# Kernel optimization log

Hardware: AMD Instinct MI355X
Metric: run time of the kernel (lower is better)

Reference implementation:

```python
import jax, jax.numpy as jnp
import numpy as np

SIGMA_AGG = 0.5
SIGMA_DIS = 3.0
ALPHA = 0.5
BETA = 0.25
EPS = 1e-5
K_MAX = 8  # number of kernel/text instances per image; labels in {0..K_MAX}, 0 = background


def setup_inputs() -> dict:
    key = jax.random.key(0)
    ks = jax.random.split(key, 7)
    B, C, H, W = 16, 4, 640, 640
    return dict(
        pred_regions=jax.random.normal(ks[0], (B, 1, H, W), jnp.float32),
        regions_gt=jax.random.randint(ks[1], (B, 1, H, W), 0, 2).astype(jnp.float32),
        pred_kernels=jax.random.normal(ks[2], (B, 1, H, W), jnp.float32),
        kernels_gt=jax.random.randint(ks[3], (B, 1, H, W), 0, 2).astype(jnp.float32),
        pred_similarities=jax.random.normal(ks[4], (B, C, H, W), jnp.float32),
        text_mask_ndi_labels=jax.random.randint(ks[5], (B, H, W), 0, K_MAX + 1, dtype=jnp.int32),
        kernel_mask_ndi_labels=jax.random.randint(ks[6], (B, H, W), 0, K_MAX + 1, dtype=jnp.int32),
    )


def _dice_loss(pred, gt, eps):
    # sigmoid -> per-sample dice, summed over batch (matches Text/KernelDiceLoss)
    p = jax.nn.sigmoid(pred).reshape(pred.shape[0], -1)
    g = gt.reshape(gt.shape[0], -1)
    inter = jnp.sum(p * g, axis=1)
    denom = (jnp.sum(p * p, axis=1) + eps) + (jnp.sum(g * g, axis=1) + eps)
    dice = (2.0 * inter + eps) / denom
    return jnp.sum(1.0 - dice)


def _agg_dis_single(sim, tlab, klab):
    # sim: (C, H, W); tlab/klab: (H, W) int instance labels (0 = background)
    C = sim.shape[0]
    sim = sim.reshape(C, -1)
    tlab = tlab.reshape(-1)
    klab = klab.reshape(-1)
    nseg = K_MAX + 1

    s2 = jnp.sum(sim * sim, axis=0)  # per-pixel squared feature norm, (N,)
    ones = jnp.ones_like(s2)
    ck = jax.ops.segment_sum(ones, klab, num_segments=nseg)  # kernel cardinalities
    ct = jax.ops.segment_sum(ones, tlab, num_segments=nseg)  # text cardinalities

    # Aggregation: || sim*1[T==i] - sim*1[K==i]/(ck_i+1) ||_F per instance i.
    # Per pixel, nonzero only for i = tlab[p] or i = klab[p]:
    inv = 1.0 / (ck + 1.0)
    same = tlab == klab
    coef_t = jnp.where(same, (1.0 - inv[klab]) ** 2, 1.0)  # contributes to instance tlab
    coef_k = jnp.where(same, 0.0, inv[klab] ** 2)          # contributes to instance klab
    n2 = (jax.ops.segment_sum(s2 * coef_t, tlab, num_segments=nseg)
          + jax.ops.segment_sum(s2 * coef_k, klab, num_segments=nseg))
    norm = jnp.sqrt(n2[1:])  # drop background segment 0
    # NOTE: torch.max(scalar, 0)[0] on a 0-d tensor is identity (no clamp) - reproduced here.
    l_agg = jnp.sum(jnp.log((norm - SIGMA_AGG) ** 2 + 1.0) / (ct[1:] + 1.0))

    # Discrimination: kernel masks are disjoint, so
    # ||mu_i - mu_j||_F^2 = a_i + a_j with a_i = sum_{K==i} s2 / (ck_i + 0.001)^2
    a = jax.ops.segment_sum(s2, klab, num_segments=nseg)[1:] / (ck[1:] + 0.001) ** 2
    pair = SIGMA_DIS - jnp.sqrt(a[:, None] + a[None, :])
    val = jnp.log(pair ** 2 + 1.0)
    triu = jnp.triu(jnp.ones((K_MAX, K_MAX), bool), 1)
    l_dis = jnp.sum(jnp.where(triu, val, 0.0)) / (K_MAX * (K_MAX - 1))
    return l_agg, l_dis


def reference(pred_regions, regions_gt, pred_kernels, kernels_gt,
              pred_similarities, text_mask_ndi_labels, kernel_mask_ndi_labels):
    # OHEM mask is computed in the torch code but never used by TextDiceLoss, so it is omitted.
    loss_regions = _dice_loss(pred_regions, regions_gt, EPS)
    loss_kernel = _dice_loss(pred_kernels, kernels_gt, EPS)
    l_agg, l_dis = jax.vmap(_agg_dis_single)(pred_similarities,
                                             text_mask_ndi_labels,
                                             kernel_mask_ndi_labels)
    loss_aggregation = jnp.sum(l_agg)
    loss_discrimination = jnp.sum(l_dis)
    loss = loss_regions + ALPHA * loss_kernel + BETA * (loss_aggregation + loss_discrimination)
    return (loss, loss_regions, loss_kernel, loss_aggregation, loss_discrimination)
```

## Files before the change

kernel.cpp:

```cpp
#include <hip/hip_runtime.h>
#include <math.h>


#define NSEG 9
#define NACC 51
#define NBATCH 16
#define EPSF 1e-5f

__device__ __forceinline__ float wave_reduce_sum(float v) {
#pragma unroll
    for (int off = 32; off > 0; off >>= 1)
        v += __shfl_down(v, off, 64);
    return v;
}

__device__ __forceinline__ float sigm(float x) {
    return 1.0f / (1.0f + __expf(-x));
}

__global__ __launch_bounds__(256) void pan_main(
    const float* __restrict__ pred_r, const float* __restrict__ gt_r,
    const float* __restrict__ pred_k, const float* __restrict__ gt_k,
    const float* __restrict__ sim,
    const int* __restrict__ tlab, const int* __restrict__ klab,
    float* __restrict__ ws, int npix)
{
    const int b = blockIdx.y;
    const int nvec = npix >> 2;
    const long long base = (long long)b * npix;
    const long long sbase = (long long)b * 4 * npix;

    const float4* pr4 = (const float4*)(pred_r + base);
    const float4* gr4 = (const float4*)(gt_r + base);
    const float4* pk4 = (const float4*)(pred_k + base);
    const float4* gk4 = (const float4*)(gt_k + base);
    const float4* c0_4 = (const float4*)(sim + sbase);
    const float4* c1_4 = (const float4*)(sim + sbase + npix);
    const float4* c2_4 = (const float4*)(sim + sbase + 2LL * npix);
    const float4* c3_4 = (const float4*)(sim + sbase + 3LL * npix);
    const int4* tl4 = (const int4*)(tlab + base);
    const int4* kl4 = (const int4*)(klab + base);

    float ctA[NSEG], ckA[NSEG], StA[NSEG], SkA[NSEG], SsA[NSEG];
#pragma unroll
    for (int s = 0; s < NSEG; ++s) {
        ctA[s] = 0.0f; ckA[s] = 0.0f; StA[s] = 0.0f; SkA[s] = 0.0f; SsA[s] = 0.0f;
    }
    float rpg = 0.0f, rpp = 0.0f, rgg = 0.0f;
    float kpg = 0.0f, kpp = 0.0f, kgg = 0.0f;

    for (int i = blockIdx.x * blockDim.x + threadIdx.x; i < nvec;
         i += gridDim.x * blockDim.x) {
        float4 pr = pr4[i], gr = gr4[i], pk = pk4[i], gk = gk4[i];
        float4 c0 = c0_4[i], c1 = c1_4[i], c2 = c2_4[i], c3 = c3_4[i];
        int4 tl = tl4[i], kl = kl4[i];

        {
            float p;
            p = sigm(pr.x); rpg += p * gr.x; rpp += p * p; rgg += gr.x * gr.x;
            p = sigm(pr.y); rpg += p * gr.y; rpp += p * p; rgg += gr.y * gr.y;
            p = sigm(pr.z); rpg += p * gr.z; rpp += p * p; rgg += gr.z * gr.z;
            p = sigm(pr.w); rpg += p * gr.w; rpp += p * p; rgg += gr.w * gr.w;
        }
        {
            float p;
            p = sigm(pk.x); kpg += p * gk.x; kpp += p * p; kgg += gk.x * gk.x;
            p = sigm(pk.y); kpg += p * gk.y; kpp += p * p; kgg += gk.y * gk.y;
            p = sigm(pk.z); kpg += p * gk.z; kpp += p * p; kgg += gk.z * gk.z;
            p = sigm(pk.w); kpg += p * gk.w; kpp += p * p; kgg += gk.w * gk.w;
        }

        float s2x = c0.x * c0.x + c1.x * c1.x + c2.x * c2.x + c3.x * c3.x;
        float s2y = c0.y * c0.y + c1.y * c1.y + c2.y * c2.y + c3.y * c3.y;
        float s2z = c0.z * c0.z + c1.z * c1.z + c2.z * c2.z + c3.z * c3.z;
        float s2w = c0.w * c0.w + c1.w * c1.w + c2.w * c2.w + c3.w * c3.w;

#pragma unroll
        for (int s = 0; s < NSEG; ++s) {
            {
                bool t = (tl.x == s), k = (kl.x == s);
                ctA[s] += t ? 1.0f : 0.0f;
                ckA[s] += k ? 1.0f : 0.0f;
                StA[s] += t ? s2x : 0.0f;
                SkA[s] += k ? s2x : 0.0f;
                SsA[s] += (t && k) ? s2x : 0.0f;
            }
            {
                bool t = (tl.y == s), k = (kl.y == s);
                ctA[s] += t ? 1.0f : 0.0f;
                ckA[s] += k ? 1.0f : 0.0f;
                StA[s] += t ? s2y : 0.0f;
                SkA[s] += k ? s2y : 0.0f;
                SsA[s] += (t && k) ? s2y : 0.0f;
            }
            {
                bool t = (tl.z == s), k = (kl.z == s);
                ctA[s] += t ? 1.0f : 0.0f;
                ckA[s] += k ? 1.0f : 0.0f;
                StA[s] += t ? s2z : 0.0f;
                SkA[s] += k ? s2z : 0.0f;
                SsA[s] += (t && k) ? s2z : 0.0f;
            }
            {
                bool t = (tl.w == s), k = (kl.w == s);
                ctA[s] += t ? 1.0f : 0.0f;
                ckA[s] += k ? 1.0f : 0.0f;
                StA[s] += t ? s2w : 0.0f;
                SkA[s] += k ? s2w : 0.0f;
                SsA[s] += (t && k) ? s2w : 0.0f;
            }
        }
    }

    __shared__ float red[4][NACC];
    const int lane = threadIdx.x & 63;
    const int wv = threadIdx.x >> 6;

#pragma unroll
    for (int s = 0; s < NSEG; ++s) {
        float r;
        r = wave_reduce_sum(ctA[s]); if (lane == 0) red[wv][s] = r;
        r = wave_reduce_sum(ckA[s]); if (lane == 0) red[wv][NSEG + s] = r;
        r = wave_reduce_sum(StA[s]); if (lane == 0) red[wv][2 * NSEG + s] = r;
        r = wave_reduce_sum(SkA[s]); if (lane == 0) red[wv][3 * NSEG + s] = r;
        r = wave_reduce_sum(SsA[s]); if (lane == 0) red[wv][4 * NSEG + s] = r;
    }
    {
        float r;
        r = wave_reduce_sum(rpg); if (lane == 0) red[wv][45] = r;
        r = wave_reduce_sum(rpp); if (lane == 0) red[wv][46] = r;
        r = wave_reduce_sum(rgg); if (lane == 0) red[wv][47] = r;
        r = wave_reduce_sum(kpg); if (lane == 0) red[wv][48] = r;
        r = wave_reduce_sum(kpp); if (lane == 0) red[wv][49] = r;
        r = wave_reduce_sum(kgg); if (lane == 0) red[wv][50] = r;
    }
    __syncthreads();
    if (threadIdx.x < NACC) {
        float s = red[0][threadIdx.x] + red[1][threadIdx.x] +
                  red[2][threadIdx.x] + red[3][threadIdx.x];
        atomicAdd(&ws[b * NACC + threadIdx.x], s);
    }
}

__global__ __launch_bounds__(64) void pan_finalize(
    const float* __restrict__ ws, float* __restrict__ out)
{
    const int b = threadIdx.x;
    float dice_r = 0.0f, dice_k = 0.0f, lagg = 0.0f, ldis = 0.0f;

    if (b < NBATCH) {
        const float* w = ws + b * NACC;
        {
            float pg = w[45], pp = w[46], gg = w[47];
            dice_r = 1.0f - (2.0f * pg + EPSF) / ((pp + EPSF) + (gg + EPSF));
            pg = w[48]; pp = w[49]; gg = w[50];
            dice_k = 1.0f - (2.0f * pg + EPSF) / ((pp + EPSF) + (gg + EPSF));
        }
        float a[8];
#pragma unroll
        for (int i = 1; i < NSEG; ++i) {
            float ct = w[i], ck = w[NSEG + i];
            float St = w[2 * NSEG + i], Sk = w[3 * NSEG + i], Ss = w[4 * NSEG + i];
            float inv = 1.0f / (ck + 1.0f);
            float omi = 1.0f - inv;
            float n2 = omi * omi * Ss + (St - Ss) + inv * inv * (Sk - Ss);
            float nrm = sqrtf(n2);
            float d = nrm - 0.5f;
            lagg += logf(d * d + 1.0f) / (ct + 1.0f);
            float ckd = ck + 0.001f;
            a[i - 1] = Sk / (ckd * ckd);
        }
#pragma unroll
        for (int i = 0; i < 8; ++i) {
#pragma unroll
            for (int j = i + 1; j < 8; ++j) {
                float pair = 3.0f - sqrtf(a[i] + a[j]);
                ldis += logf(pair * pair + 1.0f);
            }
        }
        ldis *= (1.0f / 56.0f);
    }

    dice_r = wave_reduce_sum(dice_r);
    dice_k = wave_reduce_sum(dice_k);
    lagg = wave_reduce_sum(lagg);
    ldis = wave_reduce_sum(ldis);

    if (threadIdx.x == 0) {
        float loss = dice_r + 0.5f * dice_k + 0.25f * (lagg + ldis);
        out[0] = loss;
        out[1] = dice_r;
        out[2] = dice_k;
        out[3] = lagg;
        out[4] = ldis;
    }
}

extern "C" void kernel_launch(void* const* d_in, const int* in_sizes, int n_in,
                              void* d_out, int out_size, void* d_ws, size_t ws_size,
                              hipStream_t stream) {
    const float* pred_r = (const float*)d_in[0];
    const float* gt_r   = (const float*)d_in[1];
    const float* pred_k = (const float*)d_in[2];
    const float* gt_k   = (const float*)d_in[3];
    const float* sim    = (const float*)d_in[4];
    const int*   tlab   = (const int*)d_in[5];
    const int*   klab   = (const int*)d_in[6];
    float* out = (float*)d_out;
    float* ws  = (float*)d_ws;

    const int npix = in_sizes[0] / NBATCH;

    hipMemsetAsync(ws, 0, NBATCH * NACC * sizeof(float), stream);

    dim3 grid(128, NBATCH);
    pan_main<<<grid, 256, 0, stream>>>(pred_r, gt_r, pred_k, gt_k, sim,
                                       tlab, klab, ws, npix);
    pan_finalize<<<1, 64, 0, stream>>>(ws, out);
}
```

Measured before the change: 288.5 us.

## Replace per-segment register accumulation with per-thread LDS histogram bins

Drops the unrolled nine-segment compare-and-select loop that updated 45 register accumulators for every pixel. Each pixel now does five indexed atomic adds into a per-thread column of a 45×256 shared-memory bin array. The bins are reduced per wave at the end and added straight into the workspace. The grid x-dimension also drops from 128 to 100 blocks per image. This cuts the per-pixel ALU work and register pressure, but each block now uses about 46 KB of LDS, which limits how many blocks fit on a CU and adds LDS atomic traffic.

```diff
diff --git a/kernel.cpp b/kernel.cpp
--- a/kernel.cpp
+++ b/kernel.cpp
@@ -6,6 +6,7 @@
 #define NACC 51
 #define NBATCH 16
 #define EPSF 1e-5f
+#define GX 100
 
 __device__ __forceinline__ float wave_reduce_sum(float v) {
 #pragma unroll
@@ -25,7 +26,16 @@
     const int* __restrict__ tlab, const int* __restrict__ klab,
     float* __restrict__ ws, int npix)
 {
+    __shared__ float bins[45 * 256];
+
+    const int tid = threadIdx.x;
     const int b = blockIdx.y;
+
+#pragma unroll
+    for (int q = 0; q < 45; ++q)
+        bins[q * 256 + tid] = 0.0f;
+    __syncthreads();
+
     const int nvec = npix >> 2;
     const long long base = (long long)b * npix;
     const long long sbase = (long long)b * 4 * npix;
@@ -41,15 +51,21 @@
     const int4* tl4 = (const int4*)(tlab + base);
     const int4* kl4 = (const int4*)(klab + base);
 
-    float ctA[NSEG], ckA[NSEG], StA[NSEG], SkA[NSEG], SsA[NSEG];
-#pragma unroll
-    for (int s = 0; s < NSEG; ++s) {
-        ctA[s] = 0.0f; ckA[s] = 0.0f; StA[s] = 0.0f; SkA[s] = 0.0f; SsA[s] = 0.0f;
-    }
     float rpg = 0.0f, rpp = 0.0f, rgg = 0.0f;
     float kpg = 0.0f, kpp = 0.0f, kgg = 0.0f;
 
-    for (int i = blockIdx.x * blockDim.x + threadIdx.x; i < nvec;
+#define DO_PIX(TL, KL, S2) {                                   \
+        float s2m = ((TL) == (KL)) ? (S2) : 0.0f;              \
+        float* bt = bins + (TL) * 256 + tid;                   \
+        float* bk = bins + (KL) * 256 + tid;                   \
+        atomicAdd(bt, 1.0f);                         \
+        atomicAdd(bk + 9 * 256, 1.0f);               \
+        atomicAdd(bt + 18 * 256, (S2));              \
+        atomicAdd(bk + 27 * 256, (S2));              \
+        atomicAdd(bt + 36 * 256, s2m);               \
+    }
+
+    for (int i = blockIdx.x * blockDim.x + tid; i < nvec;
          i += gridDim.x * blockDim.x) {
         float4 pr = pr4[i], gr = gr4[i], pk = pk4[i], gk = gk4[i];
         float4 c0 = c0_4[i], c1 = c1_4[i], c2 = c2_4[i], c3 = c3_4[i];
@@ -61,9 +77,6 @@
             p = sigm(pr.y); rpg += p * gr.y; rpp += p * p; rgg += gr.y * gr.y;
             p = sigm(pr.z); rpg += p * gr.z; rpp += p * p; rgg += gr.z * gr.z;
             p = sigm(pr.w); rpg += p * gr.w; rpp += p * p; rgg += gr.w * gr.w;
-        }
-        {
-            float p;
             p = sigm(pk.x); kpg += p * gk.x; kpp += p * p; kgg += gk.x * gk.x;
             p = sigm(pk.y); kpg += p * gk.y; kpp += p * p; kgg += gk.y * gk.y;
             p = sigm(pk.z); kpg += p * gk.z; kpp += p * p; kgg += gk.z * gk.z;
@@ -75,71 +88,32 @@
         float s2z = c0.z * c0.z + c1.z * c1.z + c2.z * c2.z + c3.z * c3.z;
         float s2w = c0.w * c0.w + c1.w * c1.w + c2.w * c2.w + c3.w * c3.w;
 
-#pragma unroll
-        for (int s = 0; s < NSEG; ++s) {
-            {
-                bool t = (tl.x == s), k = (kl.x == s);
-                ctA[s] += t ? 1.0f : 0.0f;
-                ckA[s] += k ? 1.0f : 0.0f;
-                StA[s] += t ? s2x : 0.0f;
-                SkA[s] += k ? s2x : 0.0f;
-                SsA[s] += (t && k) ? s2x : 0.0f;
-            }
-            {
-                bool t = (tl.y == s), k = (kl.y == s);
-                ctA[s] += t ? 1.0f : 0.0f;
-                ckA[s] += k ? 1.0f : 0.0f;
-                StA[s] += t ? s2y : 0.0f;
-                SkA[s] += k ? s2y : 0.0f;
-                SsA[s] += (t && k) ? s2y : 0.0f;
-            }
-            {
-                bool t = (tl.z == s), k = (kl.z == s);
-                ctA[s] += t ? 1.0f : 0.0f;
-                ckA[s] += k ? 1.0f : 0.0f;
-                StA[s] += t ? s2z : 0.0f;
-                SkA[s] += k ? s2z : 0.0f;
-                SsA[s] += (t && k) ? s2z : 0.0f;
-            }
-            {
-                bool t = (tl.w == s), k = (kl.w == s);
-                ctA[s] += t ? 1.0f : 0.0f;
-                ckA[s] += k ? 1.0f : 0.0f;
-                StA[s] += t ? s2w : 0.0f;
-                SkA[s] += k ? s2w : 0.0f;
-                SsA[s] += (t && k) ? s2w : 0.0f;
-            }
-        }
+        DO_PIX(tl.x, kl.x, s2x);
+        DO_PIX(tl.y, kl.y, s2y);
+        DO_PIX(tl.z, kl.z, s2z);
+        DO_PIX(tl.w, kl.w, s2w);
+    }
+#undef DO_PIX
+
+    __syncthreads();
+
+    const int lane = tid & 63;
+    const int wv = tid >> 6;
+
+    for (int q = wv; q < 45; q += 4) {
+        const float4 v = *(const float4*)&bins[q * 256 + (lane << 2)];
+        float s = (v.x + v.y) + (v.z + v.w);
+        s = wave_reduce_sum(s);
+        if (lane == 0) atomicAdd(&ws[b * NACC + q], s);
     }
 
-    __shared__ float red[4][NACC];
-    const int lane = threadIdx.x & 63;
-    const int wv = threadIdx.x >> 6;
-
-#pragma unroll
-    for (int s = 0; s < NSEG; ++s) {
-        float r;
-        r = wave_reduce_sum(ctA[s]); if (lane == 0) red[wv][s] = r;
-        r = wave_reduce_sum(ckA[s]); if (lane == 0) red[wv][NSEG + s] = r;
-        r = wave_reduce_sum(StA[s]); if (lane == 0) red[wv][2 * NSEG + s] = r;
-        r = wave_reduce_sum(SkA[s]); if (lane == 0) red[wv][3 * NSEG + s] = r;
-        r = wave_reduce_sum(SsA[s]); if (lane == 0) red[wv][4 * NSEG + s] = r;
-    }
-    {
-        float r;
-        r = wave_reduce_sum(rpg); if (lane == 0) red[wv][45] = r;
-        r = wave_reduce_sum(rpp); if (lane == 0) red[wv][46] = r;
-        r = wave_reduce_sum(rgg); if (lane == 0) red[wv][47] = r;
-        r = wave_reduce_sum(kpg); if (lane == 0) red[wv][48] = r;
-        r = wave_reduce_sum(kpp); if (lane == 0) red[wv][49] = r;
-        r = wave_reduce_sum(kgg); if (lane == 0) red[wv][50] = r;
-    }
-    __syncthreads();
-    if (threadIdx.x < NACC) {
-        float s = red[0][threadIdx.x] + red[1][threadIdx.x] +
-                  red[2][threadIdx.x] + red[3][threadIdx.x];
-        atomicAdd(&ws[b * NACC + threadIdx.x], s);
-    }
+    float r;
+    r = wave_reduce_sum(rpg); if (lane == 0) atomicAdd(&ws[b * NACC + 45], r);
+    r = wave_reduce_sum(rpp); if (lane == 0) atomicAdd(&ws[b * NACC + 46], r);
+    r = wave_reduce_sum(rgg); if (lane == 0) atomicAdd(&ws[b * NACC + 47], r);
+    r = wave_reduce_sum(kpg); if (lane == 0) atomicAdd(&ws[b * NACC + 48], r);
+    r = wave_reduce_sum(kpp); if (lane == 0) atomicAdd(&ws[b * NACC + 49], r);
+    r = wave_reduce_sum(kgg); if (lane == 0) atomicAdd(&ws[b * NACC + 50], r);
 }
 
 __global__ __launch_bounds__(64) void pan_finalize(
@@ -213,7 +187,7 @@
 
     hipMemsetAsync(ws, 0, NBATCH * NACC * sizeof(float), stream);
 
-    dim3 grid(128, NBATCH);
+    dim3 grid(GX, NBATCH);
     pan_main<<<grid, 256, 0, stream>>>(pred_r, gt_r, pred_k, gt_k, sim,
                                        tlab, klab, ws, npix);
     pan_finalize<<<1, 64, 0, stream>>>(ws, out);
```

Measured after the change: 480.1 us. 66.4% more time.
